# Kernel tuning notes

Hardware: AMD Instinct MI355X
Metric: run time of the kernel (lower is better)

Reference implementation:

```python
import jax, jax.numpy as jnp
import numpy as np

S, I, CM, C, D, CZ = 128, 512, 256, 32, 32, 128
EPS = 1e-5


def setup_inputs() -> dict:
    key = jax.random.key(0)
    ks = jax.random.split(key, 7)
    x = jax.random.normal(ks[0], (1, S, I, CM), dtype=jnp.float32)
    norm_w = 1.0 + 0.1 * jax.random.normal(ks[1], (CM,), dtype=jnp.float32)
    norm_b = 0.1 * jax.random.normal(ks[2], (CM,), dtype=jnp.float32)
    Wa = jax.random.normal(ks[3], (C, CM), dtype=jnp.float32) / np.sqrt(CM)
    Wb = jax.random.normal(ks[4], (D, CM), dtype=jnp.float32) / np.sqrt(CM)
    Wo = jax.random.normal(ks[5], (CZ, C * D), dtype=jnp.float32) / np.sqrt(C * D)
    bo = 0.1 * jax.random.normal(ks[6], (CZ,), dtype=jnp.float32)
    return {"x": x, "norm_w": norm_w, "norm_b": norm_b, "Wa": Wa, "Wb": Wb, "Wo": Wo, "bo": bo}


def reference(x, norm_w, norm_b, Wa, Wb, Wo, bo):
    m = x[0]                                   # [S, I, CM] (drop leading batch dim)
    mu = jnp.mean(m, axis=-1, keepdims=True)
    var = jnp.mean((m - mu) ** 2, axis=-1, keepdims=True)
    ln = (m - mu) * jax.lax.rsqrt(var + EPS) * norm_w + norm_b
    a = jnp.einsum('sim,cm->sic', ln, Wa)      # [S, I, C]
    b = jnp.einsum('sjm,dm->sjd', ln, Wb)      # [S, J, D]
    s = a.shape[0]
    # outer product mean over S: [I, J, C, D]; flatten order is (c, d) -> c*D + d,
    # matching the reshape(chunk, C, J, D) -> permute(0,2,1,3) -> flatten in the original.
    o = jnp.einsum('sic,sjd->ijcd', a, b) * (1.0 / s)
    z = o.reshape(o.shape[0], o.shape[1], C * D) @ Wo.T + bo  # [I, J, CZ]
    return z[None]                             # [1, I, J, CZ]
```

## Files before the change

kernel.cpp:

```cpp
#include <hip/hip_runtime.h>

#define EPS 1e-5f

typedef _Float16 half8 __attribute__((ext_vector_type(8)));
typedef _Float16 half4 __attribute__((ext_vector_type(4)));
typedef float f32x4 __attribute__((ext_vector_type(4)));

#define AB_STRIDE 72
#define AB_CHUNK  (16384 * AB_STRIDE)

__device__ __forceinline__ void load16_to_lds(const void* g, void* l) {
    __builtin_amdgcn_global_load_lds((__attribute__((address_space(1))) void*)g,
                                     (__attribute__((address_space(3))) void*)l, 16, 0, 0);
}

__global__ __launch_bounds__(256)
void k_cvt(const float* __restrict__ Wo, const float* __restrict__ Wa,
           const float* __restrict__ Wb, _Float16* __restrict__ WoH,
           _Float16* __restrict__ WabH)
{
    __shared__ _Float16 tile[32 * 36];
    const int t = threadIdx.x;
    if (blockIdx.x < 128) {
        const int n = blockIdx.x;
        float4 v = *(const float4*)(Wo + (size_t)n * 1024 + t * 4);
        int c  = t >> 3;
        int d0 = (t * 4) & 31;
        tile[(d0 + 0) * 36 + c] = (_Float16)v.x;
        tile[(d0 + 1) * 36 + c] = (_Float16)v.y;
        tile[(d0 + 2) * 36 + c] = (_Float16)v.z;
        tile[(d0 + 3) * 36 + c] = (_Float16)v.w;
        __syncthreads();
        int d  = t >> 3;
        int c0 = (t * 4) & 31;
        half4 o = *(const half4*)(tile + d * 36 + c0);
        *(half4*)(WoH + (size_t)n * 1024 + t * 4) = o;
    } else {
        int idx = ((blockIdx.x - 128) * 256 + t) * 4;
        const float* src = (idx < 8192) ? (Wa + idx) : (Wb + (idx - 8192));
        float4 v = *(const float4*)src;
        half4 h;
        h[0] = (_Float16)v.x; h[1] = (_Float16)v.y; h[2] = (_Float16)v.z; h[3] = (_Float16)v.w;
        *(half4*)(WabH + idx) = h;
    }
}

__global__ __launch_bounds__(512, 4)
void k1_ln_proj(const float* __restrict__ x, const float* __restrict__ nw,
                const float* __restrict__ nb, const _Float16* __restrict__ WabH,
                _Float16* __restrict__ aT, _Float16* __restrict__ bT)
{
    __shared__ float    xraw[3 * 8 * 256];
    __shared__ _Float16 xln[64 * 264];
    __shared__ _Float16 oT[256 * 40];

    const int tid  = threadIdx.x;
    const int lane = tid & 63;
    const int w    = tid >> 6;
    const int quad = lane >> 4;
    const int l15  = lane & 15;
    const int i0   = (blockIdx.x >> 2) * 4;
    const int sc   = blockIdx.x & 3;

    const int mt  = w & 3;
    const int ntg = w >> 2;

    const float4 gw = ((const float4*)nw)[lane];
    const float4 gb = ((const float4*)nb)[lane];

    auto src_of = [&](int c) -> const float* {
        int rl = ((c & 7) << 3) + w;
        int s_ = sc * 32 + ((c >> 3) << 4) + (rl >> 2);
        int i_ = i0 + (rl & 3);
        return x + ((size_t)s_ * 512 + i_) * 256;
    };

    load16_to_lds(src_of(0) + lane * 4, xraw + (0 * 8 + w) * 256 + lane * 4);
    load16_to_lds(src_of(1) + lane * 4, xraw + (1 * 8 + w) * 256 + lane * 4);

    int rb = 0;
    for (int half = 0; half < 2; ++half) {
        for (int cc = 0; cc < 8; ++cc) {
            const int c = half * 8 + cc;
            if (c == 15) asm volatile("s_waitcnt vmcnt(0)" ::: "memory");
            else         asm volatile("s_waitcnt vmcnt(1)" ::: "memory");

            const float4 v = *(const float4*)(xraw + (rb * 8 + w) * 256 + lane * 4);
            float sum = v.x + v.y + v.z + v.w;
            float ss  = v.x * v.x + v.y * v.y + v.z * v.z + v.w * v.w;
            #pragma unroll
            for (int off = 32; off > 0; off >>= 1) {
                sum += __shfl_xor(sum, off);
                ss  += __shfl_xor(ss, off);
            }
            float mu  = sum * (1.f / 256.f);
            float var = ss * (1.f / 256.f) - mu * mu;
            float rs  = rsqrtf(var + EPS);
            half4 o;
            o[0] = (_Float16)((v.x - mu) * rs * gw.x + gb.x);
            o[1] = (_Float16)((v.y - mu) * rs * gw.y + gb.y);
            o[2] = (_Float16)((v.z - mu) * rs * gw.z + gb.z);
            o[3] = (_Float16)((v.w - mu) * rs * gw.w + gb.w);
            int rl = (cc << 3) + w;
            *(half4*)(xln + rl * 264 + lane * 4) = o;

            if (c + 2 < 16) {
                int nb3 = rb + 2; if (nb3 >= 3) nb3 -= 3;
                load16_to_lds(src_of(c + 2) + lane * 4, xraw + (nb3 * 8 + w) * 256 + lane * 4);
            }
            ++rb; if (rb == 3) rb = 0;
        }
        asm volatile("s_waitcnt lgkmcnt(0)" ::: "memory");
        __builtin_amdgcn_s_barrier();

        f32x4 acc2[2] = {};
        #pragma unroll
        for (int kk = 0; kk < 8; ++kk) {
            half8 af = *(const half8*)(xln + (mt * 16 + l15) * 264 + kk * 32 + quad * 8);
            #pragma unroll
            for (int t = 0; t < 2; ++t) {
                half8 bf = *(const half8*)(WabH + (ntg * 32 + t * 16 + l15) * 256 + kk * 32 + quad * 8);
                acc2[t] = __builtin_amdgcn_mfma_f32_16x16x32_f16(af, bf, acc2[t], 0, 0, 0);
            }
        }

        #pragma unroll
        for (int t = 0; t < 2; ++t) {
            int c64  = ntg * 32 + t * 16 + l15;
            int base = ((c64 >= 32) ? 128 : 0) + (c64 & 31);
            int s_l  = half * 16 + mt * 4 + quad;
            #pragma unroll
            for (int r = 0; r < 4; ++r)
                oT[(base + r * 32) * 40 + s_l] = (_Float16)acc2[t][r];
        }
        asm volatile("s_waitcnt lgkmcnt(0)" ::: "memory");
        __builtin_amdgcn_s_barrier();
    }

    #pragma unroll
    for (int it2 = 0; it2 < 2; ++it2) {
        int u   = it2 * 512 + tid;
        int row = u >> 2;
        int off = (u & 3) * 8;
        half8 v = *(const half8*)(oT + row * 40 + off);
        _Float16* dst = (row < 128) ? aT : bT;
        int grow = i0 * 32 + (row & 127);
        *(half8*)(dst + (size_t)(sc >> 1) * AB_CHUNK + (size_t)grow * 72 + (sc & 1) * 32 + off) = v;
    }
}

__global__ __launch_bounds__(512, 4)
void k2_main(const _Float16* __restrict__ aT, const _Float16* __restrict__ bT,
             const _Float16* __restrict__ WoH, const float* __restrict__ bo,
             float* __restrict__ out)
{
    __shared__ _Float16 smem[33024];
    _Float16* sA = smem;
    _Float16* sB = smem + 256 * AB_STRIDE;
    _Float16* oL = smem;

    const int tid  = threadIdx.x;
    const int lane = tid & 63;
    const int w    = tid >> 6;
    const int quad = lane >> 4;
    const int l15  = lane & 15;
    const int wy   = w >> 1, wx = w & 1;

    const int jt = blockIdx.x, it = blockIdx.y;
    const char* gA = (const char*)(aT + (size_t)it * 256 * AB_STRIDE);
    const char* gB = (const char*)(bT + (size_t)jt * 128 * AB_STRIDE);

    f32x4 acc[4][4] = {};

    for (int ck = 0; ck < 2; ++ck) {
        const char* cA = gA + (size_t)ck * (AB_CHUNK * 2);
        const char* cB = gB + (size_t)ck * (AB_CHUNK * 2);
        for (int seg = w; seg < 54; seg += 8) {
            if (seg < 36) load16_to_lds(cA + seg * 1024 + lane * 16, (char*)sA + seg * 1024 + lane * 16);
            else          load16_to_lds(cB + (seg - 36) * 1024 + lane * 16, (char*)sB + (seg - 36) * 1024 + lane * 16);
        }
        __syncthreads();

        #pragma unroll
        for (int kloc = 0; kloc < 2; ++kloc) {
            half8 af[4], bf[4];
            #pragma unroll
            for (int mt = 0; mt < 4; ++mt)
                af[mt] = *(const half8*)(sA + (wy * 64 + mt * 16 + l15) * AB_STRIDE + kloc * 32 + quad * 8);
            #pragma unroll
            for (int nt = 0; nt < 4; ++nt)
                bf[nt] = *(const half8*)(sB + (wx * 64 + nt * 16 + l15) * AB_STRIDE + kloc * 32 + quad * 8);
            #pragma unroll
            for (int mt = 0; mt < 4; ++mt)
                #pragma unroll
                for (int nt = 0; nt < 4; ++nt)
                    acc[mt][nt] = __builtin_amdgcn_mfma_f32_16x16x32_f16(af[mt], bf[nt], acc[mt][nt], 0, 0, 0);
        }
        __syncthreads();
    }

    #pragma unroll
    for (int mt = 0; mt < 4; ++mt) {
        int c0     = (mt & 1) * 16 + quad * 4;
        int chunk3 = (c0 >> 3);
        int il     = wy * 2 + (mt >> 1);
        #pragma unroll
        for (int nt = 0; nt < 4; ++nt) {
            int d    = (nt & 1) * 16 + l15;
            int jl   = wx * 2 + (nt >> 1);
            int pair = il * 4 + jl;
            int cS   = (c0 & 7) + ((chunk3 ^ ((d >> 1) & 3)) << 3);
            half4 v;
            v[0] = (_Float16)(acc[mt][nt][0] * (1.f / 128.f));
            v[1] = (_Float16)(acc[mt][nt][1] * (1.f / 128.f));
            v[2] = (_Float16)(acc[mt][nt][2] * (1.f / 128.f));
            v[3] = (_Float16)(acc[mt][nt][3] * (1.f / 128.f));
            *(half4*)(oL + pair * 1032 + d * 32 + cS) = v;
        }
    }
    __syncthreads();

    f32x4 zacc[2] = {};
    const int n0 = w * 16 + l15;
    #pragma unroll 4
    for (int kk = 0; kk < 32; ++kk) {
        int csw = (quad ^ ((kk >> 1) & 3)) * 8;
        half8 oa0 = *(const half8*)(oL + (l15) * 1032 + kk * 32 + csw);
        half8 oa1 = *(const half8*)(oL + (16 + l15) * 1032 + kk * 32 + csw);
        half8 w0  = *(const half8*)(WoH + (size_t)n0 * 1024 + kk * 32 + quad * 8);
        zacc[0] = __builtin_amdgcn_mfma_f32_16x16x32_f16(oa0, w0, zacc[0], 0, 0, 0);
        zacc[1] = __builtin_amdgcn_mfma_f32_16x16x32_f16(oa1, w0, zacc[1], 0, 0, 0);
    }

    float bias = bo[w * 16 + l15];
    #pragma unroll
    for (int mt2 = 0; mt2 < 2; ++mt2) {
        #pragma unroll
        for (int r = 0; r < 4; ++r) {
            int il = mt2 * 4 + quad;
            int jl = r;
            out[(((size_t)(it * 8 + il)) * 512 + jt * 4 + jl) * 128 + w * 16 + l15] = zacc[mt2][r] + bias;
        }
    }
}

extern "C" void kernel_launch(void* const* d_in, const int* in_sizes, int n_in,
                              void* d_out, int out_size, void* d_ws, size_t ws_size,
                              hipStream_t stream)
{
    const float* x      = (const float*)d_in[0];
    const float* norm_w = (const float*)d_in[1];
    const float* norm_b = (const float*)d_in[2];
    const float* Wa     = (const float*)d_in[3];
    const float* Wb     = (const float*)d_in[4];
    const float* Wo     = (const float*)d_in[5];
    const float* bo     = (const float*)d_in[6];
    float* out = (float*)d_out;

    _Float16* aT   = (_Float16*)d_ws;
    _Float16* bT   = aT + 2 * (size_t)AB_CHUNK;
    _Float16* WoH  = bT + 2 * (size_t)AB_CHUNK;
    _Float16* WabH = WoH + 131072;

    k_cvt<<<144, 256, 0, stream>>>(Wo, Wa, Wb, WoH, WabH);
    k1_ln_proj<<<512, 512, 0, stream>>>(x, norm_w, norm_b, WabH, aT, bT);
    k2_main<<<dim3(128, 64), 512, 0, stream>>>(aT, bT, WoH, bo, out);
}
```

Before: 485.8 us.

## Halve k2 block tile to 128x128 with 256 threads and XCD-aware block mapping

Shrinks the main outer-product kernel block from 512 threads and a 256x128 (i,j) tile to 256 threads and a 128x128 tile. This halves shared memory per block and doubles the grid to 16384 one-dimensional blocks. Block indices are remapped so that each XCD covers a contiguous region of i/j tiles, to improve L2 locality of the aT/bT and Wo reads. Each wave now computes two 16-column output halves of the Wo projection instead of two row groups. In exchange, each loaded A tile is reused across fewer j values and Wo is re-read more often per output.

```diff
diff --git a/kernel.cpp b/kernel.cpp
--- a/kernel.cpp
+++ b/kernel.cpp
@@ -149,14 +149,14 @@
     }
 }
 
-__global__ __launch_bounds__(512, 4)
+__global__ __launch_bounds__(256, 4)
 void k2_main(const _Float16* __restrict__ aT, const _Float16* __restrict__ bT,
              const _Float16* __restrict__ WoH, const float* __restrict__ bo,
              float* __restrict__ out)
 {
-    __shared__ _Float16 smem[33024];
+    __shared__ _Float16 smem[18432];
     _Float16* sA = smem;
-    _Float16* sB = smem + 256 * AB_STRIDE;
+    _Float16* sB = smem + 128 * AB_STRIDE;
     _Float16* oL = smem;
 
     const int tid  = threadIdx.x;
@@ -166,8 +166,16 @@
     const int l15  = lane & 15;
     const int wy   = w >> 1, wx = w & 1;
 
-    const int jt = blockIdx.x, it = blockIdx.y;
-    const char* gA = (const char*)(aT + (size_t)it * 256 * AB_STRIDE);
+    const int wid = blockIdx.x;
+    const int xcd = wid & 7;
+    const int loc = wid >> 3;
+    const int it  = (xcd >> 2) * 64 + (loc >> 5);
+    const int jt  = (xcd & 3) * 32 + (loc & 31);
+
+    const float b0 = bo[w * 32 + l15];
+    const float b1 = bo[w * 32 + 16 + l15];
+
+    const char* gA = (const char*)(aT + (size_t)it * 128 * AB_STRIDE);
     const char* gB = (const char*)(bT + (size_t)jt * 128 * AB_STRIDE);
 
     f32x4 acc[4][4] = {};
@@ -175,9 +183,9 @@
     for (int ck = 0; ck < 2; ++ck) {
         const char* cA = gA + (size_t)ck * (AB_CHUNK * 2);
         const char* cB = gB + (size_t)ck * (AB_CHUNK * 2);
-        for (int seg = w; seg < 54; seg += 8) {
-            if (seg < 36) load16_to_lds(cA + seg * 1024 + lane * 16, (char*)sA + seg * 1024 + lane * 16);
-            else          load16_to_lds(cB + (seg - 36) * 1024 + lane * 16, (char*)sB + (seg - 36) * 1024 + lane * 16);
+        for (int seg = w; seg < 36; seg += 4) {
+            if (seg < 18) load16_to_lds(cA + seg * 1024 + lane * 16, (char*)sA + seg * 1024 + lane * 16);
+            else          load16_to_lds(cB + (seg - 18) * 1024 + lane * 16, (char*)sB + (seg - 18) * 1024 + lane * 16);
         }
         __syncthreads();
 
@@ -221,25 +229,25 @@
     __syncthreads();
 
     f32x4 zacc[2] = {};
-    const int n0 = w * 16 + l15;
-    #pragma unroll 4
-    for (int kk = 0; kk < 32; ++kk) {
-        int csw = (quad ^ ((kk >> 1) & 3)) * 8;
-        half8 oa0 = *(const half8*)(oL + (l15) * 1032 + kk * 32 + csw);
-        half8 oa1 = *(const half8*)(oL + (16 + l15) * 1032 + kk * 32 + csw);
-        half8 w0  = *(const half8*)(WoH + (size_t)n0 * 1024 + kk * 32 + quad * 8);
-        zacc[0] = __builtin_amdgcn_mfma_f32_16x16x32_f16(oa0, w0, zacc[0], 0, 0, 0);
-        zacc[1] = __builtin_amdgcn_mfma_f32_16x16x32_f16(oa1, w0, zacc[1], 0, 0, 0);
-    }
-
-    float bias = bo[w * 16 + l15];
-    #pragma unroll
-    for (int mt2 = 0; mt2 < 2; ++mt2) {
+    const _Float16* oaB = oL + l15 * 1032;
+    #pragma unroll
+    for (int h = 0; h < 2; ++h) {
+        const _Float16* woB = WoH + (size_t)(w * 32 + h * 16 + l15) * 1024;
+        #pragma unroll 4
+        for (int kk = 0; kk < 32; ++kk) {
+            int csw = (quad ^ ((kk >> 1) & 3)) * 8;
+            half8 oa = *(const half8*)(oaB + kk * 32 + csw);
+            half8 w0 = *(const half8*)(woB + kk * 32 + quad * 8);
+            zacc[h] = __builtin_amdgcn_mfma_f32_16x16x32_f16(oa, w0, zacc[h], 0, 0, 0);
+        }
+    }
+
+    #pragma unroll
+    for (int h = 0; h < 2; ++h) {
         #pragma unroll
         for (int r = 0; r < 4; ++r) {
-            int il = mt2 * 4 + quad;
-            int jl = r;
-            out[(((size_t)(it * 8 + il)) * 512 + jt * 4 + jl) * 128 + w * 16 + l15] = zacc[mt2][r] + bias;
+            out[(((size_t)(it * 4 + quad)) * 512 + jt * 4 + r) * 128 + w * 32 + h * 16 + l15]
+                = zacc[h][r] + (h ? b1 : b0);
         }
     }
 }
@@ -264,5 +272,5 @@
 
     k_cvt<<<144, 256, 0, stream>>>(Wo, Wa, Wb, WoH, WabH);
     k1_ln_proj<<<512, 512, 0, stream>>>(x, norm_w, norm_b, WabH, aT, bT);
-    k2_main<<<dim3(128, 64), 512, 0, stream>>>(aT, bT, WoH, bo, out);
-}
+    k2_main<<<16384, 256, 0, stream>>>(aT, bT, WoH, bo, out);
+}
```

After: 722.5 us. +48.7%, slower.
